# Performance work log

Measured on AMD Instinct MI355X. Metric: run time of the kernel, lower is better.

The kernel has to match this reference:

```python
import jax, jax.numpy as jnp
import numpy as np

B, C, W, H = 4, 256, 64, 64
N = W * H
SCALE = 0.02  # keep QK^T energies in a stable softmax range


def setup_inputs() -> dict:
    key = jax.random.key(0)
    ks = jax.random.split(key, 8)
    return {
        "x": jax.random.normal(ks[0], (B, C, W, H), jnp.float32),
        "geo_embed": jax.random.normal(ks[1], (B, N, C), jnp.float32),
        "Wq": jax.random.normal(ks[2], (C, C), jnp.float32) * SCALE,
        "bq": jnp.zeros((C,), jnp.float32),
        "Wk": jax.random.normal(ks[3], (C, C), jnp.float32) * SCALE,
        "bk": jnp.zeros((C,), jnp.float32),
        "Wv": jax.random.normal(ks[4], (C, C), jnp.float32) * SCALE,
        "bv": jnp.zeros((C,), jnp.float32),
        "Wgp": jax.random.normal(ks[5], (C, C), jnp.float32) * SCALE,
        "bgp": jnp.zeros((C,), jnp.float32),
        "Wgg": jax.random.normal(ks[6], (1, 2 * C), jnp.float32) * SCALE,
        "bgg": jnp.zeros((1,), jnp.float32),
    }


def reference(x, geo_embed, Wq, bq, Wk, bk, Wv, bv, Wgp, bgp, Wgg, bgg):
    b, c, w, h = x.shape
    n = w * h
    xf = x.reshape(b, c, n)  # [B, C, N]

    # 1x1 conv == per-pixel linear; q laid out [B, N, O] (permuted in torch)
    q = jnp.einsum("oc,bcn->bno", Wq, xf) + bq  # [B, N, O]

    # geo gating on the query
    ge = geo_embed @ Wgp.T + bgp  # [B, N, O]
    gate = jax.nn.sigmoid(jnp.concatenate([q, ge], axis=-1) @ Wgg.T + bgg)  # [B, N, 1]
    q = q + gate * ge

    k = jnp.einsum("oc,bcn->bon", Wk, xf) + bk[:, None]  # [B, O, N]
    v = jnp.einsum("oc,bcn->bon", Wv, xf) + bv[:, None]  # [B, C, N]

    energy = jnp.einsum("bno,bom->bnm", q, k)  # [B, N, N]
    attention = jax.nn.softmax(energy, axis=-1)

    # out = bmm(value, attention^T): out[b,c,m] = sum_n v[b,c,n] * attention[b,m,n]
    out = jnp.einsum("bcn,bmn->bcm", v, attention).reshape(b, c, w, h)

    # output gating: torch .view reinterpretation of (B, N, O) as (B, C, W, H)
    ge_r = ge.reshape(b, c, w, h)
    out = out * (1.0 + jax.nn.sigmoid(ge_r))
    return out, attention
```

## Files before the change

kernel.cpp:

```cpp
#include <hip/hip_runtime.h>
#include <hip/hip_bf16.h>
#include <math.h>

static constexpr int BB = 4;
static constexpr int CC = 256;
static constexpr int NN = 4096;

using bf16   = __bf16;
using f16    = _Float16;
using bf16x8 = __attribute__((ext_vector_type(8))) __bf16;
using bf16x4 = __attribute__((ext_vector_type(4))) __bf16;
using f16x8  = __attribute__((ext_vector_type(8))) _Float16;
using f16x4  = __attribute__((ext_vector_type(4))) _Float16;
using f32x4  = __attribute__((ext_vector_type(4))) float;

__device__ inline void gload_lds16(const void* g, void* l) {
  __builtin_amdgcn_global_load_lds(
      (const __attribute__((address_space(1))) void*)g,
      (__attribute__((address_space(3))) void*)l, 16, 0, 0);
}

__device__ inline void swz_bid(int& xb, int& yb, int& zb) {
  int gx = gridDim.x, gy = gridDim.y;
  int nwg = gx * gy * (int)gridDim.z;
  int flat = blockIdx.x + gx * (blockIdx.y + gy * blockIdx.z);
  int q = nwg >> 3;
  int w = (flat & 7) * q + (flat >> 3);
  xb = w % gx;
  int r = w / gx;
  yb = r % gy;
  zb = r / gy;
}

__global__ __launch_bounds__(256) void cvt_weights_kernel(
    const float* __restrict__ w0, const float* __restrict__ w1,
    const float* __restrict__ w2, const float* __restrict__ w3,
    bf16* __restrict__ out) {
  const float* srcs[4] = {w0, w1, w2, w3};
  const float* s = srcs[blockIdx.y];
  bf16* dst = out + (size_t)blockIdx.y * (CC * CC);
  int i = (blockIdx.x * 256 + threadIdx.x) * 4;
  float4 v = *(const float4*)(s + i);
  bf16x4 t;
  t[0] = (bf16)v.x; t[1] = (bf16)v.y; t[2] = (bf16)v.z; t[3] = (bf16)v.w;
  *(bf16x4*)(dst + i) = t;
}

__global__ __launch_bounds__(256) void cvt_f32_bf16_kernel(
    const float* __restrict__ in, bf16* __restrict__ out, long n) {
  long i = ((long)blockIdx.x * blockDim.x + threadIdx.x) * 4;
  if (i >= n) return;
  float4 v = *(const float4*)(in + i);
  bf16x4 t;
  t[0] = (bf16)v.x; t[1] = (bf16)v.y; t[2] = (bf16)v.z; t[3] = (bf16)v.w;
  *(bf16x4*)(out + i) = t;
}

__global__ __launch_bounds__(256) void transpose_x_kernel(
    const float* __restrict__ x, bf16* __restrict__ xt) {
  __shared__ float tile[64][65];
  int b  = blockIdx.z;
  int c0 = blockIdx.x * 64;
  int n0 = blockIdx.y * 64;
  const float* xp = x  + (long)b * CC * NN;
  bf16*       xtp = xt + (long)b * NN * CC;
  int tj = threadIdx.x & 63;
  int ti = threadIdx.x >> 6;
#pragma unroll
  for (int p = 0; p < 16; ++p) {
    int i = ti + p * 4;
    tile[i][tj] = xp[(long)(c0 + i) * NN + n0 + tj];
  }
  __syncthreads();
#pragma unroll
  for (int p = 0; p < 16; ++p) {
    int i = ti + p * 4;
    xtp[(long)(n0 + i) * CC + c0 + tj] = (bf16)tile[tj][i];
  }
}

__global__ __launch_bounds__(256) void proj_all_kernel(
    const bf16* __restrict__ xt, const bf16* __restrict__ geob,
    const bf16* __restrict__ Wall,
    const float* __restrict__ bq, const float* __restrict__ bgp,
    const float* __restrict__ bk, const float* __restrict__ bv,
    bf16* __restrict__ qn, float* __restrict__ ge,
    bf16* __restrict__ kn, bf16* __restrict__ vb) {
  __shared__ bf16 As[128 * 32];
  __shared__ bf16 Bs[128 * 32];
  const long NCst = (long)NN * CC;
  const int bz = blockIdx.z;
  const int b = bz >> 2, p = bz & 3;
  const bf16 *Ap, *Bp;
  const float* bias;
  int row0, col0;
  if (p == 3) {
    Ap = Wall + 2 * CC * CC;
    Bp = xt + b * NCst;
    bias = bv;
    row0 = blockIdx.x * 128;
    col0 = blockIdx.y * 128;
  } else {
    Ap = (p == 1 ? geob : xt) + b * NCst;
    Bp = Wall + (size_t)(p == 0 ? 0 : (p == 1 ? 3 : 1)) * CC * CC;
    bias = (p == 0 ? bq : (p == 1 ? bgp : bk));
    row0 = blockIdx.y * 128;
    col0 = blockIdx.x * 128;
  }

  const int t   = threadIdx.x;
  const int wid = t >> 6;
  const int l   = t & 63;
  const int lr  = l & 15;
  const int lk  = (l >> 4) * 8;
  const int warow = (wid >> 1) * 64;
  const int wbcol = (wid & 1) * 64;
  const int srow = t >> 2;
  const int scol = (t & 3) * 8;

  f32x4 acc[4][4];
#pragma unroll
  for (int i = 0; i < 4; ++i)
#pragma unroll
    for (int j = 0; j < 4; ++j) acc[i][j] = {0.f, 0.f, 0.f, 0.f};

  for (int k0 = 0; k0 < CC; k0 += 32) {
    __syncthreads();
#pragma unroll
    for (int q = 0; q < 2; ++q)
      gload_lds16(Ap + (long)(row0 + srow + 64 * q) * CC + k0 + scol,
                  As + ((q * 256 + t) * 8));
#pragma unroll
    for (int q = 0; q < 2; ++q)
      gload_lds16(Bp + (long)(col0 + srow + 64 * q) * CC + k0 + scol,
                  Bs + ((q * 256 + t) * 8));
    __syncthreads();
    bf16x8 a[4], bb[4];
#pragma unroll
    for (int i = 0; i < 4; ++i)
      a[i] = *(const bf16x8*)(As + (warow + 16 * i + lr) * 32 + lk);
#pragma unroll
    for (int j = 0; j < 4; ++j)
      bb[j] = *(const bf16x8*)(Bs + (wbcol + 16 * j + lr) * 32 + lk);
#pragma unroll
    for (int i = 0; i < 4; ++i)
#pragma unroll
      for (int j = 0; j < 4; ++j)
        acc[i][j] = __builtin_amdgcn_mfma_f32_16x16x32_bf16(a[i], bb[j], acc[i][j], 0, 0, 0);
  }

  const int orow = (l >> 4) * 4;
  const int ocol = l & 15;
#pragma unroll
  for (int i = 0; i < 4; ++i) {
#pragma unroll
    for (int j = 0; j < 4; ++j) {
      int colb = col0 + wbcol + 16 * j + ocol;
#pragma unroll
      for (int r = 0; r < 4; ++r) {
        int row = row0 + warow + 16 * i + orow + r;
        if (p == 3) {
          float vv = acc[i][j][r] + bias[row];
          vb[b * NCst + (long)row * NN + colb] = (bf16)vv;
        } else {
          float vv = acc[i][j][r] + bias[colb];
          long di = b * NCst + (long)row * CC + colb;
          if (p == 1)
            ge[di] = vv;
          else
            (p == 0 ? qn : kn)[di] = (bf16)vv;
        }
      }
    }
  }
}

template <int BIAS_MODE, int B_MODE, int OUT_MODE, bool GATE_EPI, bool SWZ>
__global__ __launch_bounds__(256) void gemm_nt_lds(
    const bf16* __restrict__ A, const void* __restrict__ Bm,
    const float* __restrict__ bias, void* __restrict__ D,
    const float* __restrict__ gefl,
    int Ncols, int K, long sA, long sB, long sD, long sGe) {
  __shared__ bf16 As[128 * 32];
  __shared__ bf16 Bs[128 * 32];
  int bx = blockIdx.x, by = blockIdx.y, bz = blockIdx.z;
  if constexpr (SWZ) swz_bid(bx, by, bz);
  const bf16* Ab = A + (long)bz * sA;
  const float* geb = GATE_EPI ? (gefl + bz * sGe) : nullptr;

  const int t   = threadIdx.x;
  const int wid = t >> 6;
  const int l   = t & 63;
  const int lr  = l & 15;
  const int lk  = (l >> 4) * 8;
  const int row0 = by * 128;
  const int col0 = bx * 128;
  const int warow = (wid >> 1) * 64;
  const int wbcol = (wid & 1) * 64;

  const int srow = t >> 2;
  const int scol = (t & 3) * 8;
  const int frow = t >> 3;
  const int fc4  = (t & 7) * 4;

  f32x4 acc[4][4];
#pragma unroll
  for (int i = 0; i < 4; ++i)
#pragma unroll
    for (int j = 0; j < 4; ++j) acc[i][j] = {0.f, 0.f, 0.f, 0.f};

  for (int k0 = 0; k0 < K; k0 += 32) {
    __syncthreads();
#pragma unroll
    for (int p = 0; p < 2; ++p)
      gload_lds16(Ab + (long)(row0 + srow + 64 * p) * K + k0 + scol,
                  As + ((p * 256 + t) * 8));
    if constexpr (B_MODE == 0) {
      const bf16* Bb = (const bf16*)Bm + (long)bz * sB;
#pragma unroll
      for (int p = 0; p < 2; ++p)
        gload_lds16(Bb + (long)(col0 + srow + 64 * p) * K + k0 + scol,
                    Bs + ((p * 256 + t) * 8));
    } else {
      const float* Bf = (const float*)Bm + (long)bz * sB;
#pragma unroll
      for (int p = 0; p < 4; ++p) {
        float4 u = *(const float4*)(Bf + (long)(col0 + frow + 32 * p) * K + k0 + fc4);
        bf16x4 tv;
        tv[0] = (bf16)u.x; tv[1] = (bf16)u.y; tv[2] = (bf16)u.z; tv[3] = (bf16)u.w;
        *(bf16x4*)(Bs + (frow + 32 * p) * 32 + fc4) = tv;
      }
    }
    __syncthreads();
    bf16x8 a[4], bb[4];
#pragma unroll
    for (int i = 0; i < 4; ++i)
      a[i] = *(const bf16x8*)(As + (warow + 16 * i + lr) * 32 + lk);
#pragma unroll
    for (int j = 0; j < 4; ++j)
      bb[j] = *(const bf16x8*)(Bs + (wbcol + 16 * j + lr) * 32 + lk);
#pragma unroll
    for (int i = 0; i < 4; ++i)
#pragma unroll
      for (int j = 0; j < 4; ++j)
        acc[i][j] = __builtin_amdgcn_mfma_f32_16x16x32_bf16(a[i], bb[j], acc[i][j], 0, 0, 0);
  }

  const int orow = (l >> 4) * 4;
  const int ocol = l & 15;
#pragma unroll
  for (int i = 0; i < 4; ++i) {
#pragma unroll
    for (int j = 0; j < 4; ++j) {
      int colb = col0 + wbcol + 16 * j + ocol;
#pragma unroll
      for (int r = 0; r < 4; ++r) {
        int row = row0 + warow + 16 * i + orow + r;
        float vv = acc[i][j][r];
        if constexpr (BIAS_MODE == 1) vv += bias[colb];
        if constexpr (BIAS_MODE == 2) vv += bias[row];
        if constexpr (GATE_EPI) {
          float g = geb[(long)row * 4096 + colb];
          vv *= 1.f + 1.f / (1.f + __expf(-g));
        }
        long di = bz * sD + (long)row * Ncols + colb;
        if constexpr (OUT_MODE == 0)
          ((float*)D)[di] = vv;
        else if constexpr (OUT_MODE == 1)
          ((bf16*)D)[di] = (bf16)vv;
        else
          ((f16*)D)[di] = (f16)vv;
      }
    }
  }
}

__global__ __launch_bounds__(256) void rowstat_kernel(
    const f16* __restrict__ e, float2* __restrict__ minv) {
  long row = blockIdx.x;
  const f16* pe = e + row * 4096;
  int t = threadIdx.x;
  __shared__ float red[8];
  float v[16];
  f16x8 e0 = *(const f16x8*)(pe + t * 16);
  f16x8 e1 = *(const f16x8*)(pe + t * 16 + 8);
#pragma unroll
  for (int i = 0; i < 8; ++i) { v[i] = (float)e0[i]; v[8 + i] = (float)e1[i]; }
  float mx = v[0];
#pragma unroll
  for (int i = 1; i < 16; ++i) mx = fmaxf(mx, v[i]);
#pragma unroll
  for (int m = 32; m >= 1; m >>= 1) mx = fmaxf(mx, __shfl_xor(mx, m, 64));
  if ((t & 63) == 0) red[t >> 6] = mx;
  __syncthreads();
  mx = fmaxf(fmaxf(red[0], red[1]), fmaxf(red[2], red[3]));
  float sum = 0.f;
#pragma unroll
  for (int i = 0; i < 16; ++i) sum += __expf(v[i] - mx);
#pragma unroll
  for (int m = 32; m >= 1; m >>= 1) sum += __shfl_xor(sum, m, 64);
  if ((t & 63) == 0) red[4 + (t >> 6)] = sum;
  __syncthreads();
  if (t == 0) {
    float s = red[4] + red[5] + red[6] + red[7];
    minv[row] = make_float2(mx, 1.f / s);
  }
}

template <bool SWZ>
__global__ __launch_bounds__(512) void pv_fused_kernel(
    const bf16* __restrict__ V, const f16* __restrict__ E,
    const float2* __restrict__ minv, float* __restrict__ attn,
    float* __restrict__ out, const float* __restrict__ ge) {
  __shared__ bf16 As[256 * 32];
  __shared__ bf16 Bs[64 * 32];
  int bx = blockIdx.x, by = blockIdx.y, bz = blockIdx.z;
  if constexpr (SWZ) swz_bid(bx, by, bz);
  const long NCst = (long)NN * CC;
  const long NNst = (long)NN * NN;
  const bf16* Vb = V + bz * NCst;
  const f16*  Eb = E + bz * NNst;
  float* Ab_attn = attn + bz * NNst;
  const float* geb = ge + bz * NCst;
  float* ob = out + bz * NCst;
  const int col0 = bx * 64;

  const int t   = threadIdx.x;
  const int wid = t >> 6;
  const int l   = t & 63;
  const int lr  = l & 15;
  const int lk  = (l >> 4) * 8;
  const int wrow = wid * 32;

  const int srow = t >> 2;
  const int scol = (t & 3) * 8;
  const int erow = t >> 3;
  const int ec4  = (t & 7) * 4;

  const float2 mi = minv[(long)bz * NN + col0 + erow];

  f32x4 acc[2][4];
#pragma unroll
  for (int i = 0; i < 2; ++i)
#pragma unroll
    for (int j = 0; j < 4; ++j) acc[i][j] = {0.f, 0.f, 0.f, 0.f};

  for (int k0 = 0; k0 < NN; k0 += 32) {
    __syncthreads();
#pragma unroll
    for (int p = 0; p < 2; ++p)
      gload_lds16(Vb + (long)(srow + 128 * p) * NN + k0 + scol,
                  As + ((p * 512 + t) * 8));
    {
      f16x4 ev = *(const f16x4*)(Eb + (long)(col0 + erow) * NN + k0 + ec4);
      float4 pv;
      pv.x = __expf((float)ev[0] - mi.x) * mi.y;
      pv.y = __expf((float)ev[1] - mi.x) * mi.y;
      pv.z = __expf((float)ev[2] - mi.x) * mi.y;
      pv.w = __expf((float)ev[3] - mi.x) * mi.y;
      *(float4*)(Ab_attn + (long)(col0 + erow) * NN + k0 + ec4) = pv;
      bf16x4 pb;
      pb[0] = (bf16)pv.x; pb[1] = (bf16)pv.y;
      pb[2] = (bf16)pv.z; pb[3] = (bf16)pv.w;
      *(bf16x4*)(Bs + erow * 32 + ec4) = pb;
    }
    __syncthreads();
    bf16x8 a[2], bb[4];
#pragma unroll
    for (int i = 0; i < 2; ++i)
      a[i] = *(const bf16x8*)(As + (wrow + 16 * i + lr) * 32 + lk);
#pragma unroll
    for (int j = 0; j < 4; ++j)
      bb[j] = *(const bf16x8*)(Bs + (16 * j + lr) * 32 + lk);
#pragma unroll
    for (int i = 0; i < 2; ++i)
#pragma unroll
      for (int j = 0; j < 4; ++j)
        acc[i][j] = __builtin_amdgcn_mfma_f32_16x16x32_bf16(a[i], bb[j], acc[i][j], 0, 0, 0);
  }

  const int orow = (l >> 4) * 4;
  const int ocol = l & 15;
#pragma unroll
  for (int i = 0; i < 2; ++i) {
#pragma unroll
    for (int j = 0; j < 4; ++j) {
      int colb = col0 + 16 * j + ocol;
#pragma unroll
      for (int r = 0; r < 4; ++r) {
        int row = wrow + 16 * i + orow + r;
        float g = geb[(long)row * 4096 + colb];
        float vv = acc[i][j][r] * (1.f + 1.f / (1.f + __expf(-g)));
        ob[(long)row * 4096 + colb] = vv;
      }
    }
  }
}

__global__ __launch_bounds__(256) void gate_kernel(
    bf16* __restrict__ q, const float* __restrict__ ge,
    const float* __restrict__ Wgg, const float* __restrict__ bgg) {
  int row = blockIdx.x * 4 + (threadIdx.x >> 6);
  int l = threadIdx.x & 63;
  bf16* qr = q + (long)row * 256;
  const float* ger = ge + (long)row * 256;
  float s = 0.f;
  float qv[4], gv[4];
#pragma unroll
  for (int i = 0; i < 4; ++i) {
    int o = l + 64 * i;
    qv[i] = (float)qr[o];
    gv[i] = ger[o];
    s += qv[i] * Wgg[o] + gv[i] * Wgg[256 + o];
  }
#pragma unroll
  for (int m = 32; m >= 1; m >>= 1) s += __shfl_xor(s, m, 64);
  float gate = 1.f / (1.f + __expf(-(s + bgg[0])));
#pragma unroll
  for (int i = 0; i < 4; ++i) {
    int o = l + 64 * i;
    qr[o] = (bf16)(qv[i] + gate * gv[i]);
  }
}

__global__ __launch_bounds__(256) void softmax32_kernel(float* __restrict__ attn) {
  long row = blockIdx.x;
  float* p = attn + row * 4096;
  int t = threadIdx.x;
  __shared__ float red[8];
  float4 v[4];
  float mx = -1e30f;
#pragma unroll
  for (int c = 0; c < 4; ++c) {
    v[c] = *(const float4*)(p + c * 1024 + t * 4);
    mx = fmaxf(mx, fmaxf(fmaxf(v[c].x, v[c].y), fmaxf(v[c].z, v[c].w)));
  }
#pragma unroll
  for (int m = 32; m >= 1; m >>= 1) mx = fmaxf(mx, __shfl_xor(mx, m, 64));
  if ((t & 63) == 0) red[t >> 6] = mx;
  __syncthreads();
  mx = fmaxf(fmaxf(red[0], red[1]), fmaxf(red[2], red[3]));
  float sum = 0.f;
#pragma unroll
  for (int c = 0; c < 4; ++c) {
    v[c].x = __expf(v[c].x - mx);
    v[c].y = __expf(v[c].y - mx);
    v[c].z = __expf(v[c].z - mx);
    v[c].w = __expf(v[c].w - mx);
    sum += v[c].x + v[c].y + v[c].z + v[c].w;
  }
#pragma unroll
  for (int m = 32; m >= 1; m >>= 1) sum += __shfl_xor(sum, m, 64);
  if ((t & 63) == 0) red[4 + (t >> 6)] = sum;
  __syncthreads();
  float inv = 1.f / (red[4] + red[5] + red[6] + red[7]);
#pragma unroll
  for (int c = 0; c < 4; ++c) {
    v[c].x *= inv; v[c].y *= inv; v[c].z *= inv; v[c].w *= inv;
    *(float4*)(p + c * 1024 + t * 4) = v[c];
  }
}

extern "C" void kernel_launch(void* const* d_in, const int* in_sizes, int n_in,
                              void* d_out, int out_size, void* d_ws, size_t ws_size,
                              hipStream_t stream) {
  const float* x    = (const float*)d_in[0];
  const float* geo  = (const float*)d_in[1];
  const float* Wq   = (const float*)d_in[2];
  const float* bq   = (const float*)d_in[3];
  const float* Wk   = (const float*)d_in[4];
  const float* bk   = (const float*)d_in[5];
  const float* Wv   = (const float*)d_in[6];
  const float* bv   = (const float*)d_in[7];
  const float* Wgp  = (const float*)d_in[8];
  const float* bgp  = (const float*)d_in[9];
  const float* Wgg  = (const float*)d_in[10];
  const float* bgg  = (const float*)d_in[11];

  float* out  = (float*)d_out;
  float* attn = out + (long)BB * CC * NN;

  char* w = (char*)d_ws;
  size_t used = 0;
  auto alloc = [&](size_t bytes) {
    char* p = w + used;
    used += (bytes + 255) & ~(size_t)255;
    return p;
  };
  bf16*  xt   = (bf16*)alloc((size_t)BB * NN * CC * 2);
  bf16*  geob = (bf16*)alloc((size_t)BB * NN * CC * 2);
  bf16*  qn   = (bf16*)alloc((size_t)BB * NN * CC * 2);
  bf16*  kn   = (bf16*)alloc((size_t)BB * NN * CC * 2);
  bf16*  vb   = (bf16*)alloc((size_t)BB * CC * NN * 2);
  float* ge   = (float*)alloc((size_t)BB * NN * CC * 4);
  bf16*  Wall = (bf16*)alloc((size_t)4 * CC * CC * 2);
  bf16*  Wvb  = Wall + 2 * CC * CC;
  size_t abf_bytes = (size_t)BB * NN * NN * 2;
  size_t minv_bytes = (size_t)BB * NN * sizeof(float2);
  bool big = (ws_size >= used + abf_bytes + minv_bytes + 512);
  f16* abf = nullptr;
  float2* minv = nullptr;
  if (big) {
    abf = (f16*)alloc(abf_bytes);
    minv = (float2*)alloc(minv_bytes);
  }

  const long NCst = (long)NN * CC;
  const long NNst = (long)NN * NN;

  cvt_weights_kernel<<<dim3(64, 4), 256, 0, stream>>>(Wq, Wk, Wv, Wgp, Wall);
  cvt_f32_bf16_kernel<<<(BB * NCst) / 1024, 256, 0, stream>>>(geo, geob, BB * NCst);
  transpose_x_kernel<<<dim3(4, 64, BB), 256, 0, stream>>>(x, xt);

  proj_all_kernel<<<dim3(2, 32, BB * 4), 256, 0, stream>>>(
      xt, geob, Wall, bq, bgp, bk, bv, qn, ge, kn, vb);
  gate_kernel<<<(BB * NN) / 4, 256, 0, stream>>>(qn, ge, Wgg, bgg);

  if (big) {
    gemm_nt_lds<0, 0, 2, false, true><<<dim3(32, 32, BB), 256, 0, stream>>>(
        qn, kn, nullptr, abf, nullptr, NN, CC, NCst, NCst, NNst, 0);
    rowstat_kernel<<<BB * NN, 256, 0, stream>>>(abf, minv);
    pv_fused_kernel<true><<<dim3(64, 1, BB), 512, 0, stream>>>(
        vb, abf, minv, attn, out, ge);
  } else {
    gemm_nt_lds<0, 0, 0, false, true><<<dim3(32, 32, BB), 256, 0, stream>>>(
        qn, kn, nullptr, attn, nullptr, NN, CC, NCst, NCst, NNst, 0);
    softmax32_kernel<<<BB * NN, 256, 0, stream>>>(attn);
    gemm_nt_lds<0, 1, 0, true, true><<<dim3(32, 2, BB), 256, 0, stream>>>(
        vb, attn, nullptr, out, ge, NN, NN, NCst, NNst, NCst, NCst);
  }
}
```

Measured before the change: 308.5 us.

## Fuse softmax row statistics into QK GEMM epilogue and retile PV kernel

The QK^T GEMM epilogue now computes per-tile row max and sum-of-exp partials into a small buffer, and a tiny reduce kernel combines them. This replaces the full re-read of the f16 energy matrix in the old rowstat kernel. The PV kernel is retiled to 256 threads with a 64-wide K step and XOR-swizzled LDS, splits channels across two blocks (doubling the grid), and prefetches the next energy chunk into registers. Splitting channels means each energy row is read and exponentiated twice, with only one split writing the attention output.

New measurement: 386.1 us. 25.2% more time.

```diff
diff --git a/kernel.cpp b/kernel.cpp
--- a/kernel.cpp
+++ b/kernel.cpp
@@ -11,7 +11,6 @@
 using bf16x8 = __attribute__((ext_vector_type(8))) __bf16;
 using bf16x4 = __attribute__((ext_vector_type(4))) __bf16;
 using f16x8  = __attribute__((ext_vector_type(8))) _Float16;
-using f16x4  = __attribute__((ext_vector_type(4))) _Float16;
 using f32x4  = __attribute__((ext_vector_type(4))) float;
 
 __device__ inline void gload_lds16(const void* g, void* l) {
@@ -175,11 +174,11 @@
   }
 }
 
-template <int BIAS_MODE, int B_MODE, int OUT_MODE, bool GATE_EPI, bool SWZ>
+template <int BIAS_MODE, int B_MODE, int OUT_MODE, bool GATE_EPI, bool SWZ, bool STAT>
 __global__ __launch_bounds__(256) void gemm_nt_lds(
     const bf16* __restrict__ A, const void* __restrict__ Bm,
     const float* __restrict__ bias, void* __restrict__ D,
-    const float* __restrict__ gefl,
+    const float* __restrict__ gefl, float2* __restrict__ pstat,
     int Ncols, int K, long sA, long sB, long sD, long sGe) {
   __shared__ bf16 As[128 * 32];
   __shared__ bf16 Bs[128 * 32];
@@ -273,71 +272,82 @@
       }
     }
   }
-}
-
-__global__ __launch_bounds__(256) void rowstat_kernel(
-    const f16* __restrict__ e, float2* __restrict__ minv) {
-  long row = blockIdx.x;
-  const f16* pe = e + row * 4096;
-  int t = threadIdx.x;
-  __shared__ float red[8];
-  float v[16];
-  f16x8 e0 = *(const f16x8*)(pe + t * 16);
-  f16x8 e1 = *(const f16x8*)(pe + t * 16 + 8);
-#pragma unroll
-  for (int i = 0; i < 8; ++i) { v[i] = (float)e0[i]; v[8 + i] = (float)e1[i]; }
-  float mx = v[0];
-#pragma unroll
-  for (int i = 1; i < 16; ++i) mx = fmaxf(mx, v[i]);
-#pragma unroll
-  for (int m = 32; m >= 1; m >>= 1) mx = fmaxf(mx, __shfl_xor(mx, m, 64));
-  if ((t & 63) == 0) red[t >> 6] = mx;
-  __syncthreads();
-  mx = fmaxf(fmaxf(red[0], red[1]), fmaxf(red[2], red[3]));
-  float sum = 0.f;
-#pragma unroll
-  for (int i = 0; i < 16; ++i) sum += __expf(v[i] - mx);
-#pragma unroll
-  for (int m = 32; m >= 1; m >>= 1) sum += __shfl_xor(sum, m, 64);
-  if ((t & 63) == 0) red[4 + (t >> 6)] = sum;
-  __syncthreads();
-  if (t == 0) {
-    float s = red[4] + red[5] + red[6] + red[7];
-    minv[row] = make_float2(mx, 1.f / s);
-  }
+
+  if constexpr (STAT) {
+    __shared__ float2 sm[128][2];
+#pragma unroll
+    for (int i = 0; i < 4; ++i) {
+#pragma unroll
+      for (int r = 0; r < 4; ++r) {
+        float m = fmaxf(fmaxf(acc[i][0][r], acc[i][1][r]),
+                        fmaxf(acc[i][2][r], acc[i][3][r]));
+#pragma unroll
+        for (int s = 8; s >= 1; s >>= 1) m = fmaxf(m, __shfl_xor(m, s, 64));
+        float sum = 0.f;
+#pragma unroll
+        for (int j = 0; j < 4; ++j) sum += __expf(acc[i][j][r] - m);
+#pragma unroll
+        for (int s = 8; s >= 1; s >>= 1) sum += __shfl_xor(sum, s, 64);
+        if ((l & 15) == 0) {
+          int Rl = warow + 16 * i + (l >> 4) * 4 + r;
+          sm[Rl][wid & 1] = make_float2(m, sum);
+        }
+      }
+    }
+    __syncthreads();
+    if (t < 128) {
+      float2 a2 = sm[t][0], b2 = sm[t][1];
+      float m = fmaxf(a2.x, b2.x);
+      float s = a2.y * __expf(a2.x - m) + b2.y * __expf(b2.x - m);
+      pstat[((long)bz * NN + row0 + t) * 32 + bx] = make_float2(m, s);
+    }
+  }
+}
+
+__global__ __launch_bounds__(256) void rowstat_reduce_kernel(
+    const float2* __restrict__ pstat, float2* __restrict__ minv) {
+  int row = blockIdx.x * 4 + (threadIdx.x >> 6);
+  int l = threadIdx.x & 63;
+  float2 v = (l < 32) ? pstat[(long)row * 32 + l] : make_float2(-1e30f, 0.f);
+  float m = v.x;
+#pragma unroll
+  for (int s = 16; s >= 1; s >>= 1) m = fmaxf(m, __shfl_xor(m, s, 64));
+  float sum = v.y * __expf(v.x - m);
+#pragma unroll
+  for (int s = 16; s >= 1; s >>= 1) sum += __shfl_xor(sum, s, 64);
+  if (l == 0) minv[row] = make_float2(m, 1.f / sum);
 }
 
 template <bool SWZ>
-__global__ __launch_bounds__(512) void pv_fused_kernel(
+__global__ __launch_bounds__(256) void pv_fused_kernel(
     const bf16* __restrict__ V, const f16* __restrict__ E,
     const float2* __restrict__ minv, float* __restrict__ attn,
     float* __restrict__ out, const float* __restrict__ ge) {
-  __shared__ bf16 As[256 * 32];
-  __shared__ bf16 Bs[64 * 32];
+  __shared__ bf16 As[128 * 64];
+  __shared__ bf16 Bs[64 * 64];
   int bx = blockIdx.x, by = blockIdx.y, bz = blockIdx.z;
   if constexpr (SWZ) swz_bid(bx, by, bz);
+  const int mrow0 = bx * 64;
+  const int ch    = by;
   const long NCst = (long)NN * CC;
   const long NNst = (long)NN * NN;
-  const bf16* Vb = V + bz * NCst;
+  const bf16* Vb = V + bz * NCst + (long)ch * 128 * NN;
   const f16*  Eb = E + bz * NNst;
-  float* Ab_attn = attn + bz * NNst;
+  float* attnb = attn + bz * NNst;
   const float* geb = ge + bz * NCst;
   float* ob = out + bz * NCst;
-  const int col0 = bx * 64;
 
   const int t   = threadIdx.x;
   const int wid = t >> 6;
   const int l   = t & 63;
   const int lr  = l & 15;
-  const int lk  = (l >> 4) * 8;
+  const int lk8 = l >> 4;
   const int wrow = wid * 32;
 
-  const int srow = t >> 2;
-  const int scol = (t & 3) * 8;
-  const int erow = t >> 3;
-  const int ec4  = (t & 7) * 4;
-
-  const float2 mi = minv[(long)bz * NN + col0 + erow];
+  const int rE = t >> 2;
+  const int cE = (t & 3) * 16;
+  const float2 mi = minv[(long)bz * NN + mrow0 + rE];
+  const f16* Erow = Eb + (long)(mrow0 + rE) * NN + cE;
 
   f32x4 acc[2][4];
 #pragma unroll
@@ -345,38 +355,66 @@
 #pragma unroll
     for (int j = 0; j < 4; ++j) acc[i][j] = {0.f, 0.f, 0.f, 0.f};
 
-  for (int k0 = 0; k0 < NN; k0 += 32) {
-    __syncthreads();
-#pragma unroll
-    for (int p = 0; p < 2; ++p)
-      gload_lds16(Vb + (long)(srow + 128 * p) * NN + k0 + scol,
-                  As + ((p * 512 + t) * 8));
+  f16x8 e0 = *(const f16x8*)(Erow);
+  f16x8 e1 = *(const f16x8*)(Erow + 8);
+
+  for (int k0 = 0; k0 < NN; k0 += 64) {
+    __syncthreads();
+    int kn = (k0 + 64 < NN) ? (k0 + 64) : 0;
+    f16x8 n0 = *(const f16x8*)(Erow + kn);
+    f16x8 n1 = *(const f16x8*)(Erow + kn + 8);
+#pragma unroll
+    for (int p = 0; p < 4; ++p) {
+      int q = p * 256 + t;
+      int r = q >> 3, c = q & 7;
+      gload_lds16(Vb + (long)r * NN + k0 + ((c ^ (r & 7)) * 8), As + q * 8);
+    }
+    float pv[16];
+#pragma unroll
+    for (int i = 0; i < 8; ++i) pv[i] = __expf((float)e0[i] - mi.x) * mi.y;
+#pragma unroll
+    for (int i = 0; i < 8; ++i) pv[8 + i] = __expf((float)e1[i] - mi.x) * mi.y;
+    if (ch == 0) {
+      float* ap = attnb + (long)(mrow0 + rE) * NN + k0 + cE;
+#pragma unroll
+      for (int c4 = 0; c4 < 4; ++c4) {
+        float4 u = {pv[4 * c4], pv[4 * c4 + 1], pv[4 * c4 + 2], pv[4 * c4 + 3]};
+        *(float4*)(ap + 4 * c4) = u;
+      }
+    }
     {
-      f16x4 ev = *(const f16x4*)(Eb + (long)(col0 + erow) * NN + k0 + ec4);
-      float4 pv;
-      pv.x = __expf((float)ev[0] - mi.x) * mi.y;
-      pv.y = __expf((float)ev[1] - mi.x) * mi.y;
-      pv.z = __expf((float)ev[2] - mi.x) * mi.y;
-      pv.w = __expf((float)ev[3] - mi.x) * mi.y;
-      *(float4*)(Ab_attn + (long)(col0 + erow) * NN + k0 + ec4) = pv;
-      bf16x4 pb;
-      pb[0] = (bf16)pv.x; pb[1] = (bf16)pv.y;
-      pb[2] = (bf16)pv.z; pb[3] = (bf16)pv.w;
-      *(bf16x4*)(Bs + erow * 32 + ec4) = pb;
-    }
-    __syncthreads();
-    bf16x8 a[2], bb[4];
-#pragma unroll
-    for (int i = 0; i < 2; ++i)
-      a[i] = *(const bf16x8*)(As + (wrow + 16 * i + lr) * 32 + lk);
-#pragma unroll
-    for (int j = 0; j < 4; ++j)
-      bb[j] = *(const bf16x8*)(Bs + (16 * j + lr) * 32 + lk);
-#pragma unroll
-    for (int i = 0; i < 2; ++i)
-#pragma unroll
-      for (int j = 0; j < 4; ++j)
-        acc[i][j] = __builtin_amdgcn_mfma_f32_16x16x32_bf16(a[i], bb[j], acc[i][j], 0, 0, 0);
+      int s = rE & 7;
+      int cc0 = (2 * (t & 3)) ^ s;
+      int cc1 = (2 * (t & 3) + 1) ^ s;
+      bf16x8 b0, b1;
+#pragma unroll
+      for (int i = 0; i < 8; ++i) { b0[i] = (bf16)pv[i]; b1[i] = (bf16)pv[8 + i]; }
+      *(bf16x8*)(Bs + rE * 64 + cc0 * 8) = b0;
+      *(bf16x8*)(Bs + rE * 64 + cc1 * 8) = b1;
+    }
+    e0 = n0; e1 = n1;
+    __syncthreads();
+#pragma unroll
+    for (int kk = 0; kk < 2; ++kk) {
+      bf16x8 a[2], bfrag[4];
+#pragma unroll
+      for (int i = 0; i < 2; ++i) {
+        int Ra = wrow + 16 * i + lr;
+        int chk = (lk8 + 4 * kk) ^ (Ra & 7);
+        a[i] = *(const bf16x8*)(As + Ra * 64 + chk * 8);
+      }
+#pragma unroll
+      for (int j = 0; j < 4; ++j) {
+        int Rb = 16 * j + lr;
+        int chk = (lk8 + 4 * kk) ^ (Rb & 7);
+        bfrag[j] = *(const bf16x8*)(Bs + Rb * 64 + chk * 8);
+      }
+#pragma unroll
+      for (int i = 0; i < 2; ++i)
+#pragma unroll
+        for (int j = 0; j < 4; ++j)
+          acc[i][j] = __builtin_amdgcn_mfma_f32_16x16x32_bf16(a[i], bfrag[j], acc[i][j], 0, 0, 0);
+    }
   }
 
   const int orow = (l >> 4) * 4;
@@ -385,13 +423,13 @@
   for (int i = 0; i < 2; ++i) {
 #pragma unroll
     for (int j = 0; j < 4; ++j) {
-      int colb = col0 + 16 * j + ocol;
+      int m = mrow0 + 16 * j + ocol;
 #pragma unroll
       for (int r = 0; r < 4; ++r) {
-        int row = wrow + 16 * i + orow + r;
-        float g = geb[(long)row * 4096 + colb];
+        int c = ch * 128 + wrow + 16 * i + orow + r;
+        float g = geb[(long)c * 4096 + m];
         float vv = acc[i][j][r] * (1.f + 1.f / (1.f + __expf(-g)));
-        ob[(long)row * 4096 + colb] = vv;
+        ob[(long)c * 4096 + m] = vv;
       }
     }
   }
@@ -495,14 +533,17 @@
   float* ge   = (float*)alloc((size_t)BB * NN * CC * 4);
   bf16*  Wall = (bf16*)alloc((size_t)4 * CC * CC * 2);
   bf16*  Wvb  = Wall + 2 * CC * CC;
-  size_t abf_bytes = (size_t)BB * NN * NN * 2;
-  size_t minv_bytes = (size_t)BB * NN * sizeof(float2);
-  bool big = (ws_size >= used + abf_bytes + minv_bytes + 512);
+  size_t abf_bytes   = (size_t)BB * NN * NN * 2;
+  size_t pstat_bytes = (size_t)BB * NN * 32 * sizeof(float2);
+  size_t minv_bytes  = (size_t)BB * NN * sizeof(float2);
+  bool big = (ws_size >= used + abf_bytes + pstat_bytes + minv_bytes + 1024);
   f16* abf = nullptr;
+  float2* pstat = nullptr;
   float2* minv = nullptr;
   if (big) {
-    abf = (f16*)alloc(abf_bytes);
-    minv = (float2*)alloc(minv_bytes);
+    abf   = (f16*)alloc(abf_bytes);
+    pstat = (float2*)alloc(pstat_bytes);
+    minv  = (float2*)alloc(minv_bytes);
   }
 
   const long NCst = (long)NN * CC;
@@ -517,16 +558,16 @@
   gate_kernel<<<(BB * NN) / 4, 256, 0, stream>>>(qn, ge, Wgg, bgg);
 
   if (big) {
-    gemm_nt_lds<0, 0, 2, false, true><<<dim3(32, 32, BB), 256, 0, stream>>>(
-        qn, kn, nullptr, abf, nullptr, NN, CC, NCst, NCst, NNst, 0);
-    rowstat_kernel<<<BB * NN, 256, 0, stream>>>(abf, minv);
-    pv_fused_kernel<true><<<dim3(64, 1, BB), 512, 0, stream>>>(
+    gemm_nt_lds<0, 0, 2, false, true, true><<<dim3(32, 32, BB), 256, 0, stream>>>(
+        qn, kn, nullptr, abf, nullptr, pstat, NN, CC, NCst, NCst, NNst, 0);
+    rowstat_reduce_kernel<<<(BB * NN) / 4, 256, 0, stream>>>(pstat, minv);
+    pv_fused_kernel<true><<<dim3(64, 2, BB), 256, 0, stream>>>(
         vb, abf, minv, attn, out, ge);
   } else {
-    gemm_nt_lds<0, 0, 0, false, true><<<dim3(32, 32, BB), 256, 0, stream>>>(
-        qn, kn, nullptr, attn, nullptr, NN, CC, NCst, NCst, NNst, 0);
+    gemm_nt_lds<0, 0, 0, false, true, false><<<dim3(32, 32, BB), 256, 0, stream>>>(
+        qn, kn, nullptr, attn, nullptr, nullptr, NN, CC, NCst, NCst, NNst, 0);
     softmax32_kernel<<<BB * NN, 256, 0, stream>>>(attn);
-    gemm_nt_lds<0, 1, 0, true, true><<<dim3(32, 2, BB), 256, 0, stream>>>(
-        vb, attn, nullptr, out, ge, NN, NN, NCst, NNst, NCst, NCst);
-  }
-}
+    gemm_nt_lds<0, 1, 0, true, true, false><<<dim3(32, 2, BB), 256, 0, stream>>>(
+        vb, attn, nullptr, out, ge, nullptr, NN, NN, NCst, NNst, NCst, NCst);
+  }
+}
```
